# Optimization experiments

Hardware: AMD Instinct MI355X
Metric: run time of the kernel (lower is better)

The kernel has to match this reference:

```python
import jax, jax.numpy as jnp
import numpy as np

B, S, SE = 4, 1024, 1024
E, H, M = 768, 12, 100
D = E // H
EPS = 1e-5
GELU_C = 0.7978845608028654  # sqrt(2/pi)


def _ln(x, g, b):
    mu = x.mean(-1, keepdims=True)
    v = ((x - mu) ** 2).mean(-1, keepdims=True)
    return g * (x - mu) / jnp.sqrt(v + EPS) + b


def _gelu(x):
    return 0.5 * x * (1.0 + jnp.tanh(GELU_C * (x + 0.044715 * x ** 3)))


def _split(x):  # [b,s,E] -> [b,H,s,D]
    b, s, _ = x.shape
    return x.reshape(b, s, H, D).transpose(0, 2, 1, 3)


def _merge(x):  # [b,H,s,D] -> [b,s,E]
    b, h, s, d = x.shape
    return x.transpose(0, 2, 1, 3).reshape(b, s, h * d)


def _forward(x, encoder_features, ln1_g, ln1_b, ln2_g, ln2_b,
             c_attn_w, c_attn_b, attn_proj_w, attn_proj_b,
             memory_features, mem_attn_w, mem_attn_b, mem_alpha_w, mem_alpha_b,
             fcq_w, fcq_b, fck_w, fck_b, fcv_w, fcv_b, enc_proj_w, enc_proj_b,
             fc_alpha1_w, fc_alpha1_b, fc_alpha2_w, fc_alpha2_b,
             mlp_fc_w, mlp_fc_b, mlp_proj_w, mlp_proj_b, mask_encoder):
    # ---- memory-augmented self-attention (note: original has NO 1/sqrt(d) scaling here) ----
    h = _ln(x, ln1_g, ln1_b)
    qkv = h @ c_attn_w + c_attn_b
    q, k, v = jnp.split(qkv, 3, axis=-1)
    q, k, v = _split(q), _split(k), _split(v)
    w = jax.nn.softmax(jnp.einsum('bhqd,bhkd->bhqk', q, k), axis=-1)
    a = _merge(jnp.einsum('bhqk,bhkd->bhqd', w, v))
    # memory slots are batch-independent -> compute once, broadcast over batch
    mem = memory_features[0] @ mem_attn_w + mem_attn_b  # [M, 2E]
    mk, mv = jnp.split(mem, 2, axis=-1)
    mk = mk.reshape(M, H, D).transpose(1, 2, 0)  # [H,D,M]
    mv = mv.reshape(M, H, D).transpose(1, 0, 2)  # [H,M,D]
    wm = jax.nn.softmax(jnp.einsum('bhqd,hdm->bhqm', q, mk), axis=-1)
    a1 = _merge(jnp.einsum('bhqm,hmd->bhqd', wm, mv))
    al = jax.nn.sigmoid(jnp.concatenate([a, a1], -1) @ mem_alpha_w + mem_alpha_b)
    a = al * a + (1.0 - al) * a1
    a = a @ attn_proj_w + attn_proj_b
    a = x + a  # residual (dropout = identity in eval)

    # ---- two cross-attentions sharing weights and ln_1 ----
    ha = _ln(a, ln1_g, ln1_b)

    def enc_dec(enc):
        qe = _split(ha @ fcq_w + fcq_b)
        ke = _split(enc @ fck_w + fck_b)
        ve = _split(enc @ fcv_w + fcv_b)
        we = jnp.einsum('bhqd,bhkd->bhqk', qe, ke) / np.float32(np.sqrt(D))
        we = jnp.where(mask_encoder, jnp.float32(-10000.0), we)
        we = jax.nn.softmax(we, axis=-1)
        o = _merge(jnp.einsum('bhqk,bhkd->bhqd', we, ve))
        return o @ enc_proj_w + enc_proj_b

    e1 = enc_dec(_ln(encoder_features[:, 0], ln1_g, ln1_b))
    e2 = enc_dec(_ln(encoder_features[:, 1], ln1_g, ln1_b))
    al1 = jax.nn.sigmoid(jnp.concatenate([a, e1], -1) @ fc_alpha1_w + fc_alpha1_b)
    al2 = jax.nn.sigmoid(jnp.concatenate([a, e2], -1) @ fc_alpha2_w + fc_alpha2_b)
    e1 = al1 * a + (1.0 - al1) * e1
    e2 = al2 * a + (1.0 - al2) * e2
    a = (e1 + e2) / np.float32(np.sqrt(2.0))

    # ---- MLP ----
    hm = _ln(a, ln2_g, ln2_b)
    m = _gelu(hm @ mlp_fc_w + mlp_fc_b) @ mlp_proj_w + mlp_proj_b
    return a + m


def setup_inputs() -> dict:
    key = jax.random.key(0)
    ks = iter(jax.random.split(key, 48))

    def rn(shape, s=0.02):
        return jax.random.normal(next(ks), shape, jnp.float32) * s

    return dict(
        x=jax.random.normal(next(ks), (B, S, E), jnp.float32),
        encoder_features=jax.random.normal(next(ks), (B, 2, SE, E), jnp.float32),
        mask_encoder=jax.random.bernoulli(next(ks), 0.1, (B, 1, 1, SE)),
        ln1_g=jnp.ones(E, jnp.float32), ln1_b=jnp.zeros(E, jnp.float32),
        ln2_g=jnp.ones(E, jnp.float32), ln2_b=jnp.zeros(E, jnp.float32),
        c_attn_w=rn((E, 3 * E)), c_attn_b=jnp.zeros(3 * E, jnp.float32),
        attn_proj_w=rn((E, E)), attn_proj_b=jnp.zeros(E, jnp.float32),
        memory_features=rn((1, M, E), 1.0),
        mem_attn_w=rn((E, 2 * E)), mem_attn_b=jnp.zeros(2 * E, jnp.float32),
        mem_alpha_w=rn((2 * E, E)), mem_alpha_b=jnp.zeros(E, jnp.float32),
        fcq_w=rn((E, E)), fcq_b=jnp.zeros(E, jnp.float32),
        fck_w=rn((E, E)), fck_b=jnp.zeros(E, jnp.float32),
        fcv_w=rn((E, E)), fcv_b=jnp.zeros(E, jnp.float32),
        enc_proj_w=rn((E, E)), enc_proj_b=jnp.zeros(E, jnp.float32),
        fc_alpha1_w=rn((2 * E, E)), fc_alpha1_b=jnp.zeros(E, jnp.float32),
        fc_alpha2_w=rn((2 * E, E)), fc_alpha2_b=jnp.zeros(E, jnp.float32),
        mlp_fc_w=rn((E, 4 * E)), mlp_fc_b=jnp.zeros(4 * E, jnp.float32),
        mlp_proj_w=rn((4 * E, E)), mlp_proj_b=jnp.zeros(E, jnp.float32),
    )


def reference(x, encoder_features, mask_encoder, ln1_g, ln1_b, ln2_g, ln2_b,
              c_attn_w, c_attn_b, attn_proj_w, attn_proj_b,
              memory_features, mem_attn_w, mem_attn_b, mem_alpha_w, mem_alpha_b,
              fcq_w, fcq_b, fck_w, fck_b, fcv_w, fcv_b, enc_proj_w, enc_proj_b,
              fc_alpha1_w, fc_alpha1_b, fc_alpha2_w, fc_alpha2_b,
              mlp_fc_w, mlp_fc_b, mlp_proj_w, mlp_proj_b):
    return _forward(x, encoder_features, ln1_g, ln1_b, ln2_g, ln2_b,
                    c_attn_w, c_attn_b, attn_proj_w, attn_proj_b,
                    memory_features, mem_attn_w, mem_attn_b, mem_alpha_w, mem_alpha_b,
                    fcq_w, fcq_b, fck_w, fck_b, fcv_w, fcv_b, enc_proj_w, enc_proj_b,
                    fc_alpha1_w, fc_alpha1_b, fc_alpha2_w, fc_alpha2_b,
                    mlp_fc_w, mlp_fc_b, mlp_proj_w, mlp_proj_b, mask_encoder)
```

## Files before the change

kernel.cpp:

```cpp
#include <hip/hip_runtime.h>

typedef __bf16 bf16_t;
typedef __bf16 bf16x8v __attribute__((ext_vector_type(8)));
typedef float f32x4 __attribute__((ext_vector_type(4)));

#define CB 4
#define CE 768
#define CH 12
#define CD 64

__device__ __forceinline__ float fexp2(float x) { return __builtin_amdgcn_exp2f(x); }

__device__ __forceinline__ void gload16(const void* g, void* l) {
    __builtin_amdgcn_global_load_lds((const __attribute__((address_space(1))) void*)g,
                                     (__attribute__((address_space(3))) void*)l, 16, 0, 0);
}

__device__ __forceinline__ void xcd_remap(int& bx, int& by, int gx, int gy) {
    int nwg = gx * gy;
    if ((nwg & 7) == 0) {
        int lin = by * gx + bx;
        int lin2 = (lin & 7) * (nwg >> 3) + (lin >> 3);
        bx = lin2 % gx;
        by = lin2 / gx;
    }
}

template<int BM, int BN, int CONCAT, int ACT, int RES, int OUT, int CMODE>
__global__ __launch_bounds__(256)
void gemm_n(const bf16_t* __restrict__ A0, const bf16_t* __restrict__ A1,
            const bf16_t* __restrict__ Bt, const float* __restrict__ bias,
            const float* __restrict__ bias2, const void* __restrict__ resid,
            void* __restrict__ C, void* __restrict__ C2, void* __restrict__ C3,
            int M, int N, int K, int lda, int ldc)
{
    constexpr int WM = BM / 2, WN = BN / 2, RM = WM / 16, RN = WN / 16;
    __shared__ __align__(16) bf16_t As0[BM * 64], As1[BM * 64];
    __shared__ __align__(16) bf16_t Bs0[BN * 64], Bs1[BN * 64];

    const int t = threadIdx.x;
    const int lane = t & 63, wave = t >> 6;
    int bx = blockIdx.x, by = blockIdx.y;
    xcd_remap(bx, by, gridDim.x, gridDim.y);
    const int m0 = by * BM, n0 = bx * BN;
    const int wm = (wave & 1) * WM, wn = (wave >> 1) * WN;
    const int fr = lane & 15, quad = lane >> 4;

    const int lr = lane >> 3;
    const int kof = ((lane & 7) ^ lr) * 8;

    const bf16_t* A1b = A1;
    if (CMODE == 6) A1b = A1 + (n0 >= 768 ? (long)4096 * 768 : 0);

    f32x4 acc[RM][RN];
#pragma unroll
    for (int i = 0; i < RM; i++)
#pragma unroll
        for (int j = 0; j < RN; j++)
#pragma unroll
            for (int p = 0; p < 4; p++) acc[i][j][p] = 0.f;

    auto stage = [&](bf16_t* As, bf16_t* Bs, int kt) {
        const bf16_t* Ab = A0;
        int kk = kt;
        if (CONCAT && kt >= 768) { Ab = A1b; kk = kt - 768; }
        const bf16_t* asrc = Ab + (long)(m0 + wave * 8 + lr) * lda + kk + kof;
#pragma unroll
        for (int c = 0; c < BM / 32; ++c)
            gload16(asrc + (long)c * 32 * lda, &As[(c * 32 + wave * 8) * 64]);
        const bf16_t* bsrc = Bt + (long)(n0 + wave * 8 + lr) * K + kt + kof;
#pragma unroll
        for (int c = 0; c < BN / 32; ++c)
            gload16(bsrc + (long)c * 32 * K, &Bs[(c * 32 + wave * 8) * 64]);
    };

    const int sw = fr & 7;
    auto compute = [&](const bf16_t* As, const bf16_t* Bs) {
        bf16x8v af[RM][2], bfr[RN][2];
        const int s0 = quad ^ sw;
#pragma unroll
        for (int i = 0; i < RM; ++i) {
            const char* rb = (const char*)As + (wm + i * 16 + fr) * 128;
            af[i][0] = *(const bf16x8v*)(rb + (s0 << 4));
            af[i][1] = *(const bf16x8v*)(rb + ((s0 ^ 4) << 4));
        }
#pragma unroll
        for (int j = 0; j < RN; ++j) {
            const char* rb = (const char*)Bs + (wn + j * 16 + fr) * 128;
            bfr[j][0] = *(const bf16x8v*)(rb + (s0 << 4));
            bfr[j][1] = *(const bf16x8v*)(rb + ((s0 ^ 4) << 4));
        }
#pragma unroll
        for (int ks = 0; ks < 2; ++ks)
#pragma unroll
            for (int i = 0; i < RM; ++i)
#pragma unroll
                for (int j = 0; j < RN; ++j)
                    acc[i][j] = __builtin_amdgcn_mfma_f32_16x16x32_bf16(af[i][ks], bfr[j][ks], acc[i][j], 0, 0, 0);
    };

    const int nk = K >> 6;
    stage(As0, Bs0, 0);
    __syncthreads();
    for (int kt = 0; kt + 2 <= nk; kt += 2) {
        stage(As1, Bs1, (kt + 1) << 6);
        compute(As0, Bs0);
        __syncthreads();
        if (kt + 2 < nk) stage(As0, Bs0, (kt + 2) << 6);
        compute(As1, Bs1);
        __syncthreads();
    }

    const int rq = quad * 4, cn = fr;
#pragma unroll
    for (int i = 0; i < RM; i++)
#pragma unroll
        for (int j = 0; j < RN; j++) {
            int col = n0 + wn + j * 16 + cn;
            int t3 = (CMODE == 4 || CMODE == 5 || CMODE == 9) ? (col / 768) : 0;
            int cc = col - t3 * 768;
            float bv = 0.f;
            if (CMODE == 5)      bv = t3 ? bias2[cc] : bias[cc];
            else if (CMODE == 6) bv = (col < 768) ? bias[col] : bias2[col - 768];
            else if (bias)       bv = bias[col];
            const int row0 = m0 + wm + i * 16 + rq;
            float vv[4];
#pragma unroll
            for (int p = 0; p < 4; p++) {
                float v = acc[i][j][p] + bv;
                if (ACT == 1) v = 1.f / (1.f + __expf(-v));
                if (ACT == 2) {
                    float u2 = 1.5957691216057308f * (v + 0.044715f * v * v * v);
                    v = v / (1.f + __expf(-u2));
                }
                if (RES == 2) v += ((const float*)resid)[(long)(row0 + p) * ldc + col];
                vv[p] = v;
            }
            if (CMODE == 0) {
#pragma unroll
                for (int p = 0; p < 4; p++) {
                    long idx = (long)(row0 + p) * ldc + col;
                    if (OUT == 0)      ((bf16_t*)C)[idx] = (bf16_t)vv[p];
                    else if (OUT == 1) ((float*)C)[idx] = vv[p];
                    else { ((float*)C)[idx] = vv[p]; ((bf16_t*)C2)[idx] = (bf16_t)vv[p]; }
                }
            } else if (CMODE == 6) {
                long base = (col < 768) ? 0 : ((long)4096 * 768 - 768);
#pragma unroll
                for (int p = 0; p < 4; p++)
                    ((bf16_t*)C)[base + (long)(row0 + p) * 768 + col] = (bf16_t)vv[p];
            } else if (CMODE == 7) {
#pragma unroll
                for (int p = 0; p < 4; p++) {
                    long idx = (long)(row0 + p) * ldc + col;
                    float a  = (float)((const bf16_t*)C2)[idx];
                    float a1 = (float)((const bf16_t*)C3)[idx];
                    ((bf16_t*)C)[idx] = (bf16_t)(vv[p] * a + (1.f - vv[p]) * a1);
                }
            } else if (CMODE == 9) {
                int hh = cc >> 6, dd = cc & 63;
                if (t3 == 0) {
#pragma unroll
                    for (int p = 0; p < 4; p++)
                        ((bf16_t*)C)[(long)hh * 8192 + (row0 + p) * 64 + dd] =
                            (row0 + p < 100) ? (bf16_t)vv[p] : (bf16_t)0.f;
                } else {
                    union { ushort4 u4; bf16_t b[4]; } pk;
#pragma unroll
                    for (int p = 0; p < 4; p++)
                        pk.b[p] = (row0 + p < 100) ? (bf16_t)vv[p] : (bf16_t)0.f;
                    *(ushort4*)((bf16_t*)C2 + (long)hh * 8192 + dd * 128 + row0) = pk.u4;
                }
            } else {
                int bb = row0 >> 10, ss0 = row0 & 1023;
                int hh = cc >> 6, dd = cc & 63;
                long srow = (long)(bb * CH + hh) * 1024 + ss0;
                long tbase = (((long)(bb * CH + hh) * 64) + dd) * 1024 + ss0;
                union { ushort4 u4; bf16_t b[4]; } pk;
#pragma unroll
                for (int p = 0; p < 4; p++) pk.b[p] = (bf16_t)vv[p];
                if (CMODE == 2) {
#pragma unroll
                    for (int p = 0; p < 4; p++)
                        ((bf16_t*)C)[(srow + p) * 64 + dd] = pk.b[p];
                } else if (CMODE == 5) {
                    if (t3 == 0) {
#pragma unroll
                        for (int p = 0; p < 4; p++)
                            ((bf16_t*)C)[(srow + p) * 64 + dd] = pk.b[p];
                    } else {
                        *(ushort4*)((bf16_t*)C2 + tbase) = pk.u4;
                    }
                } else {
                    if (t3 == 0) {
#pragma unroll
                        for (int p = 0; p < 4; p++)
                            ((bf16_t*)C)[(srow + p) * 64 + dd] = pk.b[p];
                    } else if (t3 == 1) {
#pragma unroll
                        for (int p = 0; p < 4; p++)
                            ((bf16_t*)C2)[(srow + p) * 64 + dd] = pk.b[p];
                    } else {
                        *(ushort4*)((bf16_t*)C3 + tbase) = pk.u4;
                    }
                }
            }
        }
}

template<int MODE, int QR>
__global__ __launch_bounds__(256)
void flash_attn(const bf16_t* __restrict__ Q, const bf16_t* __restrict__ K,
                const bf16_t* __restrict__ V, const bf16_t* __restrict__ K2,
                const bf16_t* __restrict__ V2, const int* __restrict__ mask,
                bf16_t* __restrict__ O)
{
    constexpr int QG = QR / 64;
    __shared__ __align__(16) bf16_t Qs[QR * 64];
    __shared__ __align__(16) bf16_t Ks0[64 * 64], Ks1[64 * 64];
    __shared__ __align__(16) bf16_t Vs[64 * 64];

    const int t = threadIdx.x;
    const int lane = t & 63, wave = t >> 6;
    int bx = blockIdx.x, bz = blockIdx.z;
    {
        int nwg = gridDim.x * gridDim.z;
        if ((nwg & 7) == 0) {
            int lin = bz * gridDim.x + bx;
            int lin2 = (lin & 7) * (nwg >> 3) + (lin >> 3);
            bx = lin2 % gridDim.x;
            bz = lin2 / gridDim.x;
        }
    }
    const bool memrole = (MODE == 3) && (bz >= 48);
    const int zq = (MODE == 1) ? (bz % 48) : (memrole ? bz - 48 : bz);
    const int b = zq / CH, h = zq % CH;
    long obase = (MODE == 1) ? (long)(bz / 48) * ((long)4096 * 768)
                             : (memrole ? (long)4096 * 768 : 0);
    const int q0 = bx * QR;

    const bf16_t* Qb = Q + (long)zq * 65536 + (long)q0 * 64;
    const bf16_t* Kb = memrole ? K2 + (long)h * 8192 : K + (long)bz * 65536;
    const bf16_t* Vb = memrole ? V2 + (long)h * 8192 : V + (long)bz * 65536;
    const int ldv = memrole ? 128 : 1024;
    const int NT = memrole ? 2 : 16;
    constexpr float SCL = (MODE == 1) ? 0.18033688011112042f : 1.4426950408889634f;

    const int lr = lane >> 3, kof = ((lane & 7) ^ lr) * 8;

    auto stageK = [&](bf16_t* Ks, int kt) {
#pragma unroll
        for (int c = 0; c < 2; ++c) {
            int r = wave * 8 + c * 32;
            gload16(Kb + (long)(kt * 64 + r + lr) * 64 + kof, &Ks[r * 64]);
        }
    };
    auto stageV = [&](int kt) {
#pragma unroll
        for (int c = 0; c < 2; ++c) {
            int r = wave * 8 + c * 32;
            gload16(Vb + (long)(r + lr) * ldv + kt * 64 + kof, &Vs[r * 64]);
        }
    };

    stageK(Ks0, 0);
#pragma unroll
    for (int c = 0; c < QR / 32; ++c) {
        int r = wave * 8 + c * 32;
        gload16(Qb + (long)(r + lr) * 64 + kof, &Qs[r * 64]);
    }
    __syncthreads();

    const int fr = lane & 15, quad = lane >> 4;
    const int sw = fr & 7;
    bf16x8v qf[QG][2];
#pragma unroll
    for (int g = 0; g < QG; g++)
#pragma unroll
        for (int ks = 0; ks < 2; ks++) {
            const char* rb = (const char*)Qs + (wave * (16 * QG) + g * 16 + fr) * 128;
            bf16x8v raw = *(const bf16x8v*)(rb + (((quad ^ sw) ^ (ks << 2)) << 4));
#pragma unroll
            for (int i = 0; i < 8; i++) qf[g][ks][i] = (bf16_t)((float)raw[i] * SCL);
        }

    bf16_t* Ps = &Qs[wave * (16 * QG) * 64];

    f32x4 o[4][QG];
    float mrow[QG], lrow[QG];
#pragma unroll
    for (int g = 0; g < QG; g++) { mrow[g] = -1e30f; lrow[g] = 0.f; }
#pragma unroll
    for (int j = 0; j < 4; j++)
#pragma unroll
        for (int g = 0; g < QG; g++)
#pragma unroll
            for (int p = 0; p < 4; p++) o[j][g][p] = 0.f;

    auto qkt_sm = [&](const bf16_t* Ks, int kt) {
        f32x4 s[4][QG];
#pragma unroll
        for (int j = 0; j < 4; j++)
#pragma unroll
            for (int g = 0; g < QG; g++)
#pragma unroll
                for (int p = 0; p < 4; p++) s[j][g][p] = 0.f;
        __builtin_amdgcn_s_setprio(1);
#pragma unroll
        for (int ks = 0; ks < 2; ks++) {
            bf16x8v bk[4];
#pragma unroll
            for (int j = 0; j < 4; j++) {
                const char* rb = (const char*)Ks + (j * 16 + fr) * 128;
                bk[j] = *(const bf16x8v*)(rb + (((quad ^ sw) ^ (ks << 2)) << 4));
            }
#pragma unroll
            for (int j = 0; j < 4; j++)
#pragma unroll
                for (int g = 0; g < QG; g++)
                    s[j][g] = __builtin_amdgcn_mfma_f32_16x16x32_bf16(bk[j], qf[g][ks], s[j][g], 0, 0, 0);
        }
        __builtin_amdgcn_s_setprio(0);
        if (MODE == 1) {
#pragma unroll
            for (int j = 0; j < 4; j++) {
                int4 mv = *(const int4*)&mask[(long)b * 1024 + kt * 64 + j * 16 + quad * 4];
#pragma unroll
                for (int g = 0; g < QG; g++) {
                    s[j][g][0] = mv.x ? -14426.95f : s[j][g][0];
                    s[j][g][1] = mv.y ? -14426.95f : s[j][g][1];
                    s[j][g][2] = mv.z ? -14426.95f : s[j][g][2];
                    s[j][g][3] = mv.w ? -14426.95f : s[j][g][3];
                }
            }
        }
        if (MODE == 3 && memrole) {
#pragma unroll
            for (int j = 0; j < 4; j++)
#pragma unroll
                for (int p = 0; p < 4; p++)
                    if (kt * 64 + j * 16 + quad * 4 + p >= 100)
#pragma unroll
                        for (int g = 0; g < QG; g++) s[j][g][p] = -1e30f;
        }
        float tmax[QG];
        bool need = false;
#pragma unroll
        for (int g = 0; g < QG; g++) {
            float tm = s[0][g][0];
#pragma unroll
            for (int j = 0; j < 4; j++)
#pragma unroll
                for (int p = 0; p < 4; p++) tm = fmaxf(tm, s[j][g][p]);
            tm = fmaxf(tm, __shfl_xor(tm, 16, 64));
            tm = fmaxf(tm, __shfl_xor(tm, 32, 64));
            tmax[g] = tm;
            need = need || (tm > mrow[g] + 8.f);
        }
        if (__any(need ? 1 : 0)) {
#pragma unroll
            for (int g = 0; g < QG; g++) {
                float mnew = fmaxf(mrow[g], tmax[g]);
                float alpha = fexp2(mrow[g] - mnew);
                lrow[g] *= alpha;
                mrow[g] = mnew;
                float arow[4];
#pragma unroll
                for (int p = 0; p < 4; p++)
                    arow[p] = __shfl(alpha, (lane & 48) | (quad * 4 + p), 64);
#pragma unroll
                for (int j = 0; j < 4; j++)
#pragma unroll
                    for (int p = 0; p < 4; p++) o[j][g][p] *= arow[p];
            }
        }
#pragma unroll
        for (int g = 0; g < QG; g++) {
            float rs = 0.f;
#pragma unroll
            for (int j = 0; j < 4; j++)
#pragma unroll
                for (int p = 0; p < 4; p++) {
                    float e = fexp2(s[j][g][p] - mrow[g]);
                    s[j][g][p] = e;
                    rs += e;
                }
            lrow[g] += rs;
        }
#pragma unroll
        for (int j = 0; j < 4; j++)
#pragma unroll
            for (int g = 0; g < QG; g++) {
                union { uint2 u; bf16_t bb[4]; } pk;
#pragma unroll
                for (int p = 0; p < 4; p++) pk.bb[p] = (bf16_t)s[j][g][p];
                int row = g * 16 + fr;
                *(uint2*)((char*)Ps + row * 128 +
                          (((j * 2 + (quad >> 1)) ^ sw) << 4) + ((quad & 1) << 3)) = pk.u;
            }
    };

    auto pv = [&]() {
        __builtin_amdgcn_s_setprio(1);
#pragma unroll
        for (int ks = 0; ks < 2; ks++) {
            bf16x8v af[QG], bv[4];
#pragma unroll
            for (int g = 0; g < QG; g++) {
                const char* rb = (const char*)Ps + (g * 16 + fr) * 128;
                af[g] = *(const bf16x8v*)(rb + (((quad ^ sw) ^ (ks << 2)) << 4));
            }
#pragma unroll
            for (int j = 0; j < 4; j++) {
                const char* rb = (const char*)Vs + (j * 16 + fr) * 128;
                bv[j] = *(const bf16x8v*)(rb + (((quad ^ sw) ^ (ks << 2)) << 4));
            }
#pragma unroll
            for (int j = 0; j < 4; j++)
#pragma unroll
                for (int g = 0; g < QG; g++)
                    o[j][g] = __builtin_amdgcn_mfma_f32_16x16x32_bf16(af[g], bv[j], o[j][g], 0, 0, 0);
        }
        __builtin_amdgcn_s_setprio(0);
    };

    for (int kt = 0; kt < NT; kt += 2) {
        stageV(kt);
        if (kt + 1 < NT) stageK(Ks1, kt + 1);
        qkt_sm(Ks0, kt);
        __syncthreads();
        pv();
        __syncthreads();
        stageV(kt + 1);
        if (kt + 2 < NT) stageK(Ks0, kt + 2);
        qkt_sm(Ks1, kt + 1);
        __syncthreads();
        pv();
        __syncthreads();
    }
#pragma unroll
    for (int g = 0; g < QG; g++) {
        lrow[g] += __shfl_xor(lrow[g], 16, 64);
        lrow[g] += __shfl_xor(lrow[g], 32, 64);
        float linv[4];
#pragma unroll
        for (int p = 0; p < 4; p++)
            linv[p] = 1.f / __shfl(lrow[g], (lane & 48) | (quad * 4 + p), 64);
#pragma unroll
        for (int p = 0; p < 4; p++) {
            int srow = q0 + wave * (16 * QG) + g * 16 + quad * 4 + p;
            long base = ((long)b * 1024 + srow) * 768 + h * 64 + obase;
#pragma unroll
            for (int j = 0; j < 4; j++)
                O[base + j * 16 + fr] = (bf16_t)(o[j][g][p] * linv[p]);
        }
    }
}

__device__ __forceinline__ void ln_vals(float v0, float v1, float v2, bf16_t* out,
                                        const float* g, const float* b,
                                        long ob, int t)
{
    __shared__ float red[4];
    float s = v0 + v1 + v2;
    for (int m = 32; m; m >>= 1) s += __shfl_xor(s, m, 64);
    if ((t & 63) == 0) red[t >> 6] = s;
    __syncthreads();
    s = red[0] + red[1] + red[2] + red[3];
    __syncthreads();
    const float mu = s * (1.f / 768.f);
    float d0 = v0 - mu, d1 = v1 - mu, d2 = v2 - mu;
    float q = d0 * d0 + d1 * d1 + d2 * d2;
    for (int m = 32; m; m >>= 1) q += __shfl_xor(q, m, 64);
    if ((t & 63) == 0) red[t >> 6] = q;
    __syncthreads();
    q = red[0] + red[1] + red[2] + red[3];
    const float rstd = rsqrtf(q * (1.f / 768.f) + 1e-5f);
    out[ob + t]       = (bf16_t)(g[t]       * d0 * rstd + b[t]);
    out[ob + t + 256] = (bf16_t)(g[t + 256] * d1 * rstd + b[t + 256]);
    out[ob + t + 512] = (bf16_t)(g[t + 512] * d2 * rstd + b[t + 512]);
}

__global__ __launch_bounds__(256)
void ln_kernel(const float* __restrict__ in, bf16_t* __restrict__ out,
               const float* __restrict__ g, const float* __restrict__ b)
{
    const int r = blockIdx.x;
    const int t = threadIdx.x;
    long base = (long)r * CE;
    ln_vals(in[base + t], in[base + t + 256], in[base + t + 512],
            out, g, b, base, t);
}

__global__ __launch_bounds__(256)
void ln_enc(const float* __restrict__ encf, bf16_t* __restrict__ out,
            const float* __restrict__ g, const float* __restrict__ b)
{
    const int r = blockIdx.x;
    const int t = threadIdx.x;
    const int e = r >> 12, rr = r & 4095, bb = rr >> 10, s = rr & 1023;
    long base = ((long)(bb * 2 + e) * 1024 + s) * CE;
    ln_vals(encf[base + t], encf[base + t + 256], encf[base + t + 512],
            out, g, b, (long)r * CE, t);
}

__global__ __launch_bounds__(256)
void fuse_gates_ln(const bf16_t* __restrict__ gal, const bf16_t* __restrict__ eo,
                   float* __restrict__ rf, bf16_t* __restrict__ out,
                   const float* __restrict__ g, const float* __restrict__ b)
{
    const long SZel = (long)4096 * 768;
    const int r = blockIdx.x, t = threadIdx.x;
    long base = (long)r * CE;
    float v[3];
#pragma unroll
    for (int k = 0; k < 3; k++) {
        long idx = base + t + k * 256;
        float g1 = (float)gal[idx], g2 = (float)gal[idx + SZel];
        float e1 = (float)eo[idx],  e2 = (float)eo[idx + SZel];
        float rr = rf[idx];
        float vv = (g1 * rr + (1.f - g1) * e1 + g2 * rr + (1.f - g2) * e2)
                   * 0.7071067811865476f;
        rf[idx] = vv;
        v[k] = vv;
    }
    ln_vals(v[0], v[1], v[2], out, g, b, base, t);
}

__global__ void zero_out(float* __restrict__ out)
{
    out[blockIdx.x * 256 + threadIdx.x] = 0.f;
}

#define NTW 12
struct TTab {
    const float* src[NTW];
    unsigned long dst[NTW];
    int kn[NTW];
    int pre[NTW + 1];
    const float* memf;
    unsigned long membOff;
};

__global__ void transpose_all(TTab tt, char* __restrict__ ws)
{
    __shared__ bf16_t tile[32][33];
    int tb = blockIdx.x;
    if (tb >= tt.pre[NTW]) {
        int idx = (tb - tt.pre[NTW]) * 256 + threadIdx.y * 32 + threadIdx.x;
        int row = idx / 768;
        ((bf16_t*)(ws + tt.membOff))[idx] =
            (row < 100) ? (bf16_t)tt.memf[idx] : (bf16_t)0.f;
        return;
    }
    int e = 0;
#pragma unroll
    for (int i = 0; i < NTW; i++) if (tb >= tt.pre[i + 1]) e = i + 1;
    int local = tb - tt.pre[e];
    const int K = tt.kn[e] >> 16, N = tt.kn[e] & 0xffff;
    const float* in = tt.src[e];
    bf16_t* out = (bf16_t*)(ws + tt.dst[e]);
    const int ntx = N / 32;
    const int n0 = (local % ntx) * 32, k0 = (local / ntx) * 32;
    int tx = threadIdx.x, ty = threadIdx.y;
    for (int i = ty; i < 32; i += 8)
        tile[i][tx] = (bf16_t)in[(long)(k0 + i) * N + n0 + tx];
    __syncthreads();
    for (int i = ty; i < 32; i += 8)
        out[(long)(n0 + i) * K + k0 + tx] = tile[tx][i];
}

extern "C" void kernel_launch(void* const* d_in, const int* in_sizes, int n_in,
                              void* d_out, int out_size, void* d_ws, size_t ws_size,
                              hipStream_t stream)
{
    (void)in_sizes; (void)n_in; (void)out_size;
    const float* x        = (const float*)d_in[0];
    const float* encf     = (const float*)d_in[1];
    const int*   maskenc  = (const int*)d_in[2];
    const float* ln1_g    = (const float*)d_in[3];
    const float* ln1_b    = (const float*)d_in[4];
    const float* ln2_g    = (const float*)d_in[5];
    const float* ln2_b    = (const float*)d_in[6];
    const float* c_attn_w = (const float*)d_in[7];
    const float* c_attn_b = (const float*)d_in[8];
    const float* aproj_w  = (const float*)d_in[9];
    const float* aproj_b  = (const float*)d_in[10];
    const float* memf     = (const float*)d_in[11];
    const float* mattn_w  = (const float*)d_in[12];
    const float* mattn_b  = (const float*)d_in[13];
    const float* malpha_w = (const float*)d_in[14];
    const float* malpha_b = (const float*)d_in[15];
    const float* fcq_w    = (const float*)d_in[16];
    const float* fcq_b    = (const float*)d_in[17];
    const float* fck_w    = (const float*)d_in[18];
    const float* fck_b    = (const float*)d_in[19];
    const float* fcv_w    = (const float*)d_in[20];
    const float* fcv_b    = (const float*)d_in[21];
    const float* eproj_w  = (const float*)d_in[22];
    const float* eproj_b  = (const float*)d_in[23];
    const float* fa1_w    = (const float*)d_in[24];
    const float* fa1_b    = (const float*)d_in[25];
    const float* fa2_w    = (const float*)d_in[26];
    const float* fa2_b    = (const float*)d_in[27];
    const float* mfc_w    = (const float*)d_in[28];
    const float* mfc_b    = (const float*)d_in[29];
    const float* mproj_w  = (const float*)d_in[30];
    const float* mproj_b  = (const float*)d_in[31];
    float* dout = (float*)d_out;

    size_t off = 0;
    auto alloc = [&](size_t bytes) -> void* {
        void* p = (char*)d_ws + off;
        off = (off + bytes + 255) & ~(size_t)255;
        return p;
    };
    const size_t SZ = (size_t)4096 * 768 * 2;
    const long SZel = (long)4096 * 768;
    bf16_t* wt_cattn  = (bf16_t*)alloc((size_t)2304 * 768 * 2);
    bf16_t* wt_aproj  = (bf16_t*)alloc((size_t)768 * 768 * 2);
    bf16_t* wt_malpha = (bf16_t*)alloc((size_t)768 * 1536 * 2);
    bf16_t* wt_fcq    = (bf16_t*)alloc((size_t)768 * 768 * 2);
    bf16_t* wt_fck    = (bf16_t*)alloc((size_t)768 * 768 * 2);
    bf16_t* wt_fcv    = (bf16_t*)alloc((size_t)768 * 768 * 2);
    bf16_t* wt_eproj  = (bf16_t*)alloc((size_t)768 * 768 * 2);
    bf16_t* wt_fa1    = (bf16_t*)alloc((size_t)768 * 1536 * 2);
    bf16_t* wt_fa2    = (bf16_t*)alloc((size_t)768 * 1536 * 2);
    bf16_t* wt_mfc    = (bf16_t*)alloc((size_t)3072 * 768 * 2);
    bf16_t* wt_mproj  = (bf16_t*)alloc((size_t)768 * 3072 * 2);
    bf16_t* wt_mattn  = (bf16_t*)alloc((size_t)1536 * 768 * 2);
    bf16_t* memb   = (bf16_t*)alloc((size_t)128 * 768 * 2);
    bf16_t* mkt    = (bf16_t*)alloc((size_t)CH * 128 * 64 * 2);
    bf16_t* mvt    = (bf16_t*)alloc((size_t)CH * 64 * 128 * 2);
    bf16_t* bufA   = (bf16_t*)alloc(SZ);
    bf16_t* qbuf   = (bf16_t*)alloc(SZ);
    bf16_t* kbuf   = (bf16_t*)alloc(2 * SZ);
    bf16_t* vtbuf  = (bf16_t*)alloc(2 * SZ);
    bf16_t* asbuf  = (bf16_t*)alloc(2 * SZ);
    bf16_t* bufB   = (bf16_t*)alloc(2 * SZ);
    float*  residf = (float*)alloc((size_t)4096 * 768 * 4);
    bf16_t* residb = (bf16_t*)alloc(SZ);

    if (off > ws_size) {
        zero_out<<<12288, 256, 0, stream>>>(dout);
        return;
    }
    bf16_t* mid = kbuf;
    bf16_t* galbuf = kbuf;
    bf16_t* eobuf = bufB;

    const dim3 blk(256);

    TTab tt;
    {
        const float* srcs[NTW] = {c_attn_w, aproj_w, malpha_w, fcq_w, fck_w, fcv_w,
                                  eproj_w, fa1_w, fa2_w, mfc_w, mproj_w, mattn_w};
        bf16_t* dsts[NTW] = {wt_cattn, wt_aproj, wt_malpha, wt_fcq, wt_fck, wt_fcv,
                             wt_eproj, wt_fa1, wt_fa2, wt_mfc, wt_mproj, wt_mattn};
        int Ks[NTW] = {768, 768, 1536, 768, 768, 768, 768, 1536, 1536, 768, 3072, 768};
        int Ns[NTW] = {2304, 768, 768, 768, 768, 768, 768, 768, 768, 3072, 768, 1536};
        int acc = 0;
        for (int i = 0; i < NTW; i++) {
            tt.src[i] = srcs[i];
            tt.dst[i] = (unsigned long)((char*)dsts[i] - (char*)d_ws);
            tt.kn[i] = (Ks[i] << 16) | Ns[i];
            tt.pre[i] = acc;
            acc += (Ks[i] / 32) * (Ns[i] / 32);
        }
        tt.pre[NTW] = acc;
        tt.memf = memf;
        tt.membOff = (unsigned long)((char*)memb - (char*)d_ws);
        transpose_all<<<acc + 384, dim3(32, 8), 0, stream>>>(tt, (char*)d_ws);
    }

    gemm_n<64,64,0,0,0,0,9><<<dim3(24, 2), blk, 0, stream>>>(
        memb, nullptr, wt_mattn, mattn_b, nullptr, nullptr, mkt, mvt, nullptr,
        128, 1536, 768, 768, 1536);

    ln_kernel<<<4096, blk, 0, stream>>>(x, bufA, ln1_g, ln1_b);
    gemm_n<128,64,0,0,0,0,4><<<dim3(36, 32), blk, 0, stream>>>(
        bufA, nullptr, wt_cattn, c_attn_b, nullptr, nullptr, qbuf, kbuf, vtbuf,
        4096, 2304, 768, 768, 0);

    flash_attn<3,64><<<dim3(16, 1, 96), blk, 0, stream>>>(
        qbuf, kbuf, vtbuf, mkt, mvt, nullptr, asbuf);

    gemm_n<64,64,1,1,0,0,7><<<dim3(12, 64), blk, 0, stream>>>(
        asbuf, asbuf + SZel, wt_malpha, malpha_b, nullptr, nullptr, bufA, asbuf, asbuf + SZel,
        4096, 768, 1536, 768, 768);
    gemm_n<64,64,0,0,2,2,0><<<dim3(12, 64), blk, 0, stream>>>(
        bufA, nullptr, wt_aproj, aproj_b, nullptr, x, residf, residb, nullptr,
        4096, 768, 768, 768, 768);

    ln_kernel<<<4096, blk, 0, stream>>>(residf, bufA, ln1_g, ln1_b);
    gemm_n<64,64,0,0,0,0,2><<<dim3(12, 64), blk, 0, stream>>>(
        bufA, nullptr, wt_fcq, fcq_b, nullptr, nullptr, qbuf, nullptr, nullptr,
        4096, 768, 768, 768, 0);

    ln_enc<<<8192, blk, 0, stream>>>(encf, bufB, ln1_g, ln1_b);
    gemm_n<128,64,0,0,0,0,5><<<dim3(24, 64), blk, 0, stream>>>(
        bufB, nullptr, wt_fck, fck_b, fcv_b, nullptr, kbuf, vtbuf, nullptr,
        8192, 1536, 768, 768, 0);
    flash_attn<1,128><<<dim3(8, 1, 96), blk, 0, stream>>>(
        qbuf, kbuf, vtbuf, nullptr, nullptr, maskenc, asbuf);
    gemm_n<128,64,0,0,0,0,0><<<dim3(12, 64), blk, 0, stream>>>(
        asbuf, nullptr, wt_eproj, eproj_b, nullptr, nullptr, eobuf, nullptr, nullptr,
        8192, 768, 768, 768, 768);
    gemm_n<128,64,1,1,0,0,6><<<dim3(24, 32), blk, 0, stream>>>(
        residb, eobuf, wt_fa1, fa1_b, fa2_b, nullptr, galbuf, nullptr, nullptr,
        4096, 1536, 1536, 768, 768);
    fuse_gates_ln<<<4096, blk, 0, stream>>>(galbuf, eobuf, residf, bufA, ln2_g, ln2_b);

    gemm_n<128,64,0,2,0,0,0><<<dim3(48, 32), blk, 0, stream>>>(
        bufA, nullptr, wt_mfc, mfc_b, nullptr, nullptr, mid, nullptr, nullptr,
        4096, 3072, 768, 768, 3072);
    gemm_n<128,64,0,0,2,1,0><<<dim3(12, 32), blk, 0, stream>>>(
        mid, nullptr, wt_mproj, mproj_b, nullptr, residf, dout, nullptr, nullptr,
        4096, 768, 3072, 3072, 768);
}
```

Baseline: 536.1 us.

## Double-buffer V tiles in flash attention, merge LN launches, enlarge self-attn Q tile

Adds a second V shared-memory buffer so K and V for the next tile are prefetched together, cutting the barriers per tile pair from four to two. The self-attention launch switches from 64 to 128 query rows per block, halving the grid. The two layer-norm launches over the residual and encoder features are merged into one kernel. The extra V buffer raises LDS use, and the larger Q tile lowers parallelism for the self-attention kernel.

```diff
diff --git a/kernel.cpp b/kernel.cpp
--- a/kernel.cpp
+++ b/kernel.cpp
@@ -218,7 +218,7 @@
     constexpr int QG = QR / 64;
     __shared__ __align__(16) bf16_t Qs[QR * 64];
     __shared__ __align__(16) bf16_t Ks0[64 * 64], Ks1[64 * 64];
-    __shared__ __align__(16) bf16_t Vs[64 * 64];
+    __shared__ __align__(16) bf16_t Vs0[64 * 64], Vs1[64 * 64];
 
     const int t = threadIdx.x;
     const int lane = t & 63, wave = t >> 6;
@@ -255,7 +255,7 @@
             gload16(Kb + (long)(kt * 64 + r + lr) * 64 + kof, &Ks[r * 64]);
         }
     };
-    auto stageV = [&](int kt) {
+    auto stageV = [&](bf16_t* Vs, int kt) {
 #pragma unroll
         for (int c = 0; c < 2; ++c) {
             int r = wave * 8 + c * 32;
@@ -264,6 +264,7 @@
     };
 
     stageK(Ks0, 0);
+    stageV(Vs0, 0);
 #pragma unroll
     for (int c = 0; c < QR / 32; ++c) {
         int r = wave * 8 + c * 32;
@@ -400,7 +401,7 @@
             }
     };
 
-    auto pv = [&]() {
+    auto pv = [&](const bf16_t* Vs) {
         __builtin_amdgcn_s_setprio(1);
 #pragma unroll
         for (int ks = 0; ks < 2; ks++) {
@@ -425,17 +426,13 @@
     };
 
     for (int kt = 0; kt < NT; kt += 2) {
-        stageV(kt);
-        if (kt + 1 < NT) stageK(Ks1, kt + 1);
+        if (kt + 1 < NT) { stageK(Ks1, kt + 1); stageV(Vs1, kt + 1); }
         qkt_sm(Ks0, kt);
+        pv(Vs0);
         __syncthreads();
-        pv();
-        __syncthreads();
-        stageV(kt + 1);
-        if (kt + 2 < NT) stageK(Ks0, kt + 2);
+        if (kt + 2 < NT) { stageK(Ks0, kt + 2); stageV(Vs0, kt + 2); }
         qkt_sm(Ks1, kt + 1);
-        __syncthreads();
-        pv();
+        pv(Vs1);
         __syncthreads();
     }
 #pragma unroll
@@ -493,15 +490,22 @@
 }
 
 __global__ __launch_bounds__(256)
-void ln_enc(const float* __restrict__ encf, bf16_t* __restrict__ out,
-            const float* __restrict__ g, const float* __restrict__ b)
-{
-    const int r = blockIdx.x;
-    const int t = threadIdx.x;
-    const int e = r >> 12, rr = r & 4095, bb = rr >> 10, s = rr & 1023;
-    long base = ((long)(bb * 2 + e) * 1024 + s) * CE;
-    ln_vals(encf[base + t], encf[base + t + 256], encf[base + t + 512],
-            out, g, b, (long)r * CE, t);
+void ln_both(const float* __restrict__ residf, const float* __restrict__ encf,
+             bf16_t* __restrict__ outA, bf16_t* __restrict__ outB,
+             const float* __restrict__ g, const float* __restrict__ b)
+{
+    const int r = blockIdx.x, t = threadIdx.x;
+    if (r < 4096) {
+        long base = (long)r * CE;
+        ln_vals(residf[base + t], residf[base + t + 256], residf[base + t + 512],
+                outA, g, b, base, t);
+    } else {
+        const int rr = r - 4096;
+        const int e = rr >> 12, r2 = rr & 4095, bb = r2 >> 10, s = r2 & 1023;
+        long base = ((long)(bb * 2 + e) * 1024 + s) * CE;
+        ln_vals(encf[base + t], encf[base + t + 256], encf[base + t + 512],
+                outB, g, b, (long)rr * CE, t);
+    }
 }
 
 __global__ __launch_bounds__(256)
@@ -682,7 +686,7 @@
         bufA, nullptr, wt_cattn, c_attn_b, nullptr, nullptr, qbuf, kbuf, vtbuf,
         4096, 2304, 768, 768, 0);
 
-    flash_attn<3,64><<<dim3(16, 1, 96), blk, 0, stream>>>(
+    flash_attn<3,128><<<dim3(8, 1, 96), blk, 0, stream>>>(
         qbuf, kbuf, vtbuf, mkt, mvt, nullptr, asbuf);
 
     gemm_n<64,64,1,1,0,0,7><<<dim3(12, 64), blk, 0, stream>>>(
@@ -692,12 +696,10 @@
         bufA, nullptr, wt_aproj, aproj_b, nullptr, x, residf, residb, nullptr,
         4096, 768, 768, 768, 768);
 
-    ln_kernel<<<4096, blk, 0, stream>>>(residf, bufA, ln1_g, ln1_b);
+    ln_both<<<12288, blk, 0, stream>>>(residf, encf, bufA, bufB, ln1_g, ln1_b);
     gemm_n<64,64,0,0,0,0,2><<<dim3(12, 64), blk, 0, stream>>>(
         bufA, nullptr, wt_fcq, fcq_b, nullptr, nullptr, qbuf, nullptr, nullptr,
         4096, 768, 768, 768, 0);
-
-    ln_enc<<<8192, blk, 0, stream>>>(encf, bufB, ln1_g, ln1_b);
     gemm_n<128,64,0,0,0,0,5><<<dim3(24, 64), blk, 0, stream>>>(
         bufB, nullptr, wt_fck, fck_b, fcv_b, nullptr, kbuf, vtbuf, nullptr,
         8192, 1536, 768, 768, 0);
```

New measurement: 546.3 us. Within noise of the previous version (+1.9%).
